# Kernel tuning notes

Hardware: AMD Instinct MI355X
Metric: run time of the kernel (lower is better)

## Reference

```python
import jax, jax.numpy as jnp
import numpy as np

HIDDEN = 2048
NUM_EXPERTS = 64
TOP_K = 2


def setup_inputs() -> dict:
    key = jax.random.key(0)
    k1, k2 = jax.random.split(key)
    x = jax.random.normal(k1, (4, 4096, HIDDEN), dtype=jnp.float32)
    # nn.Linear(hidden, num_experts, bias=False): weight shape [E, H], y = x @ W.T
    W = jax.random.normal(k2, (NUM_EXPERTS, HIDDEN), dtype=jnp.float32) * (HIDDEN ** -0.5)
    return {"x": x, "W": W}


def reference(x, W):
    B, S, H = x.shape
    E, K = NUM_EXPERTS, TOP_K
    xf = x.reshape(-1, H)                       # [N, H]
    gate_logits = xf @ W.T                      # [N, E]
    routing_probs = jax.nn.softmax(gate_logits, axis=-1)
    top_k_probs, top_k_indices = jax.lax.top_k(routing_probs, K)  # [N, K]
    denom = jnp.sum(top_k_probs, axis=-1, keepdims=True) + 1e-6
    routing_weights = (top_k_probs / denom).reshape(B, S, K)
    expert_indices = top_k_indices.reshape(B, S, K)

    # aux load-balancing loss (training path)
    N = xf.shape[0]
    # expert_mask.mean(0): fraction of tokens assigned to each expert
    assign_per_expert = jnp.zeros((E,), jnp.float32).at[top_k_indices.reshape(-1)].add(1.0) / N
    prob_per_expert = jnp.mean(routing_probs, axis=0)             # [E]
    aux_loss = (jnp.sum(prob_per_expert * prob_per_expert) * E
                + jnp.sum(assign_per_expert * assign_per_expert) * E)

    # expert_counts update (bincount over selected indices)
    expert_counts = jnp.zeros((E,), jnp.float32).at[top_k_indices.reshape(-1)].add(1.0)

    return routing_weights, expert_indices, aux_loss, expert_counts
```

## Files before the change

kernel.cpp:

```cpp
#include <hip/hip_runtime.h>

#define HID 2048
#define NEXP 64
#define NTOK 16384
#define TM 32
#define NTHREADS 256
#define NCHUNK 32
#define KPH 4
#define CPW 8
#define WS_W_OFF 1024
#define CHUNK_B 24576

#define OUT_IDX_OFF (2 * NTOK)
#define OUT_AUX_OFF (4 * NTOK)
#define OUT_CNT_OFF (4 * NTOK + 1)

typedef __attribute__((ext_vector_type(8))) short bhalf8;
typedef __attribute__((ext_vector_type(16))) float f32x16;

__device__ __forceinline__ void split3(float v, unsigned short& h1, unsigned short& h2, unsigned short& h3) {
    unsigned int u = __float_as_uint(v);
    unsigned int r1 = (u + 0x7FFFu + ((u >> 16) & 1u)) & 0xFFFF0000u;
    float f1 = __uint_as_float(r1);
    float d1 = v - f1;
    unsigned int u2 = __float_as_uint(d1);
    unsigned int r2 = (u2 + 0x7FFFu + ((u2 >> 16) & 1u)) & 0xFFFF0000u;
    float f2 = __uint_as_float(r2);
    float d2 = d1 - f2;
    h1 = (unsigned short)(r1 >> 16);
    h2 = (unsigned short)(r2 >> 16);
    h3 = (unsigned short)(__float_as_uint(d2) >> 16);
}

__device__ __forceinline__ void xsplit(float4 va, float4 vb, bhalf8& o1, bhalf8& o2, bhalf8& o3) {
    float f[8] = {va.x, va.y, va.z, va.w, vb.x, vb.y, vb.z, vb.w};
    union U { bhalf8 v; unsigned int u[4]; } u1, u2, u3;
#pragma unroll
    for (int t = 0; t < 4; t++) {
        float a = f[2 * t], b = f[2 * t + 1];
        unsigned int ua = __float_as_uint(a), ub = __float_as_uint(b);
        float da = a - __uint_as_float(ua & 0xFFFF0000u);
        float db = b - __uint_as_float(ub & 0xFFFF0000u);
        unsigned int uda = __float_as_uint(da), udb = __float_as_uint(db);
        float da2 = da - __uint_as_float(uda & 0xFFFF0000u);
        float db2 = db - __uint_as_float(udb & 0xFFFF0000u);
        u1.u[t] = (ua >> 16) | (ub & 0xFFFF0000u);
        u2.u[t] = (uda >> 16) | (udb & 0xFFFF0000u);
        u3.u[t] = (__float_as_uint(da2) >> 16) | (__float_as_uint(db2) & 0xFFFF0000u);
    }
    o1 = u1.v; o2 = u2.v; o3 = u3.v;
}

__global__ __launch_bounds__(256) void wsplit_kernel(const float* __restrict__ W,
                                                     char* __restrict__ wq,
                                                     float* __restrict__ wsf) {
    if (blockIdx.x == 0 && threadIdx.x < 2 * NEXP) wsf[threadIdx.x] = 0.f;
    int idx8 = (blockIdx.x * 256 + threadIdx.x) * 8;
    int e = idx8 >> 11;
    int k0 = idx8 & 2047;
    int c = k0 >> 6, ks = (k0 >> 4) & 3, half = (k0 >> 3) & 1;
    int g = e >> 5, l = (e & 31) + 32 * half;
    const float4* wp = (const float4*)(W + (size_t)e * HID + k0);
    float4 v0 = wp[0], v1 = wp[1];
    float f[8] = {v0.x, v0.y, v0.z, v0.w, v1.x, v1.y, v1.z, v1.w};
    unsigned int p1[4], p2[4], p3[4];
#pragma unroll
    for (int t = 0; t < 4; t++) {
        unsigned short a1, a2, a3, b1, b2, b3;
        split3(f[2 * t], a1, a2, a3);
        split3(f[2 * t + 1], b1, b2, b3);
        p1[t] = (unsigned int)a1 | ((unsigned int)b1 << 16);
        p2[t] = (unsigned int)a2 | ((unsigned int)b2 << 16);
        p3[t] = (unsigned int)a3 | ((unsigned int)b3 << 16);
    }
    char* base = wq + (size_t)(((c * 4 + ks) * 3 + 0) * 2 + g) * 1024 + l * 16;
    *(uint4*)(base)        = make_uint4(p1[0], p1[1], p1[2], p1[3]);
    *(uint4*)(base + 2048) = make_uint4(p2[0], p2[1], p2[2], p2[3]);
    *(uint4*)(base + 4096) = make_uint4(p3[0], p3[1], p3[2], p3[3]);
}

__global__ __launch_bounds__(NTHREADS, 2) void router_main(
    const float* __restrict__ x, const char* __restrict__ wq,
    float* __restrict__ out, float* __restrict__ ws_accum)
{
    __shared__ float slab[KPH * TM * 68];
    __shared__ float smax[TM];
    __shared__ float sinvZ[TM];
    __shared__ float scount[NEXP];

    const int tid = threadIdx.x;
    const int w = tid >> 6;
    const int lane = tid & 63;
    const int r = lane & 31;
    const int h = lane >> 5;
    const int n0 = blockIdx.x * TM;

    const float* xrow = x + (size_t)(n0 + r) * HID + h * 8;

    f32x16 acc0, acc1;
#pragma unroll
    for (int i = 0; i < 16; i++) { acc0[i] = 0.f; acc1[i] = 0.f; }

#pragma unroll 1
    for (int i = 0; i < CPW; ++i) {
        const int c = w * CPW + i;
        const float* xc = xrow + c * 64;
        float4 pxa[4], pxb[4];
#pragma unroll
        for (int ks = 0; ks < 4; ks++) {
            pxa[ks] = *(const float4*)(xc + ks * 16);
            pxb[ks] = *(const float4*)(xc + ks * 16 + 4);
        }
        const char* wc = wq + (size_t)c * CHUNK_B + lane * 16;
#pragma unroll
        for (int ks = 0; ks < 4; ks++) {
            bhalf8 A1, A2, A3;
            xsplit(pxa[ks], pxb[ks], A1, A2, A3);
            const char* wk = wc + ks * 6144;
            {
                bhalf8 B1 = *(const bhalf8*)(wk);
                bhalf8 B2 = *(const bhalf8*)(wk + 2048);
                bhalf8 B3 = *(const bhalf8*)(wk + 4096);
                acc0 = __builtin_amdgcn_mfma_f32_32x32x16_bf16(A1, B1, acc0, 0, 0, 0);
                acc0 = __builtin_amdgcn_mfma_f32_32x32x16_bf16(A1, B2, acc0, 0, 0, 0);
                acc0 = __builtin_amdgcn_mfma_f32_32x32x16_bf16(A2, B1, acc0, 0, 0, 0);
                acc0 = __builtin_amdgcn_mfma_f32_32x32x16_bf16(A1, B3, acc0, 0, 0, 0);
                acc0 = __builtin_amdgcn_mfma_f32_32x32x16_bf16(A2, B2, acc0, 0, 0, 0);
                acc0 = __builtin_amdgcn_mfma_f32_32x32x16_bf16(A3, B1, acc0, 0, 0, 0);
            }
            {
                bhalf8 B1 = *(const bhalf8*)(wk + 1024);
                bhalf8 B2 = *(const bhalf8*)(wk + 2048 + 1024);
                bhalf8 B3 = *(const bhalf8*)(wk + 4096 + 1024);
                acc1 = __builtin_amdgcn_mfma_f32_32x32x16_bf16(A1, B1, acc1, 0, 0, 0);
                acc1 = __builtin_amdgcn_mfma_f32_32x32x16_bf16(A1, B2, acc1, 0, 0, 0);
                acc1 = __builtin_amdgcn_mfma_f32_32x32x16_bf16(A2, B1, acc1, 0, 0, 0);
                acc1 = __builtin_amdgcn_mfma_f32_32x32x16_bf16(A1, B3, acc1, 0, 0, 0);
                acc1 = __builtin_amdgcn_mfma_f32_32x32x16_bf16(A2, B2, acc1, 0, 0, 0);
                acc1 = __builtin_amdgcn_mfma_f32_32x32x16_bf16(A3, B1, acc1, 0, 0, 0);
            }
        }
    }

#pragma unroll
    for (int reg = 0; reg < 16; reg++) {
        int row = (reg & 3) + 8 * (reg >> 2) + 4 * h;
        slab[(w * TM + row) * 68 + r]      = acc0[reg];
        slab[(w * TM + row) * 68 + 32 + r] = acc1[reg];
    }
    if (tid < NEXP) scount[tid] = 0.f;
    __syncthreads();

    float* logits = slab;
#pragma unroll
    for (int idx = tid; idx < TM * NEXP; idx += NTHREADS) {
        int t = idx >> 6, e = idx & 63;
        float v = slab[(0 * TM + t) * 68 + e] + slab[(1 * TM + t) * 68 + e]
                + slab[(2 * TM + t) * 68 + e] + slab[(3 * TM + t) * 68 + e];
        logits[t * 68 + e] = v;
    }
    __syncthreads();

    if (tid < TM) {
        const int t = tid;
        float m1 = -3.4e38f, m2 = -3.4e38f;
        int i1 = 0, i2 = 0;
        for (int e = 0; e < NEXP; e++) {
            float v = logits[t * 68 + e];
            if (v > m1) { m2 = m1; i2 = i1; m1 = v; i1 = e; }
            else if (v > m2) { m2 = v; i2 = e; }
        }
        float Z = 0.f;
        for (int e = 0; e < NEXP; e++)
            Z += __expf(logits[t * 68 + e] - m1);
        float invZ = 1.f / Z;
        float p1 = invZ;
        float p2 = __expf(m2 - m1) * invZ;
        float denom = p1 + p2 + 1e-6f;
        int n = n0 + t;
        out[2 * n + 0] = p1 / denom;
        out[2 * n + 1] = p2 / denom;
        out[OUT_IDX_OFF + 2 * n + 0] = (float)i1;
        out[OUT_IDX_OFF + 2 * n + 1] = (float)i2;
        smax[t] = m1;
        sinvZ[t] = invZ;
        atomicAdd(&scount[i1], 1.f);
        atomicAdd(&scount[i2], 1.f);
    }
    __syncthreads();

    if (tid < NEXP) {
        const int e = tid;
        float s = 0.f;
        for (int t = 0; t < TM; t++)
            s += __expf(logits[t * 68 + e] - smax[t]) * sinvZ[t];
        atomicAdd(&ws_accum[e], s);
        atomicAdd(&ws_accum[NEXP + e], scount[e]);
    }
}

__global__ void router_finish(const float* __restrict__ ws_accum,
                              float* __restrict__ out)
{
    const int e = threadIdx.x;
    const float invN = 1.f / (float)NTOK;
    float p = ws_accum[e] * invN;
    float a = ws_accum[NEXP + e] * invN;
    float v = p * p + a * a;
#pragma unroll
    for (int off = 32; off > 0; off >>= 1)
        v += __shfl_down(v, off);
    if (e == 0) out[OUT_AUX_OFF] = v * (float)NEXP;
    out[OUT_CNT_OFF + e] = ws_accum[NEXP + e];
}

extern "C" void kernel_launch(void* const* d_in, const int* in_sizes, int n_in,
                              void* d_out, int out_size, void* d_ws, size_t ws_size,
                              hipStream_t stream)
{
    const float* x = (const float*)d_in[0];
    const float* W = (const float*)d_in[1];
    float* out = (float*)d_out;
    float* wsf = (float*)d_ws;
    char* wq = (char*)d_ws + WS_W_OFF;

    wsplit_kernel<<<64, 256, 0, stream>>>(W, wq, wsf);
    router_main<<<NTOK / TM, NTHREADS, 0, stream>>>(x, wq, out, wsf);
    router_finish<<<1, 64, 0, stream>>>(wsf, out);
}
```

Baseline: 217.0 us.

## Split K across 8 waves and parallelize top-2 softmax with wave shuffles

The main router kernel now runs 512 threads per block, so each of 8 waves handles 4 of the 32 K-chunks instead of 8, and launch bounds request 4 blocks per CU. This doubles the waves working on each 32-token tile to hide global-load latency. The serial per-token top-2 and softmax loop, which ran on 32 threads, is replaced by 64-lane wave-shuffle reductions, and per-expert probability sums come from shared-memory atomics. The cost is a larger shared slab and a longer cross-wave partial-sum reduction, plus possible register pressure from the tighter launch bounds. The weight-split kernel is also relaunched as 256 blocks of 64 threads.

```diff
diff --git a/kernel.cpp b/kernel.cpp
--- a/kernel.cpp
+++ b/kernel.cpp
@@ -4,10 +4,11 @@
 #define NEXP 64
 #define NTOK 16384
 #define TM 32
-#define NTHREADS 256
+#define NTHREADS 512
 #define NCHUNK 32
-#define KPH 4
-#define CPW 8
+#define KPH 8
+#define CPW 4
+#define TPW 4
 #define WS_W_OFF 1024
 #define CHUNK_B 24576
 
@@ -51,11 +52,11 @@
     o1 = u1.v; o2 = u2.v; o3 = u3.v;
 }
 
-__global__ __launch_bounds__(256) void wsplit_kernel(const float* __restrict__ W,
-                                                     char* __restrict__ wq,
-                                                     float* __restrict__ wsf) {
-    if (blockIdx.x == 0 && threadIdx.x < 2 * NEXP) wsf[threadIdx.x] = 0.f;
-    int idx8 = (blockIdx.x * 256 + threadIdx.x) * 8;
+__global__ __launch_bounds__(64) void wsplit_kernel(const float* __restrict__ W,
+                                                    char* __restrict__ wq,
+                                                    float* __restrict__ wsf) {
+    if (blockIdx.x < 2) wsf[blockIdx.x * 64 + threadIdx.x] = 0.f;
+    int idx8 = (blockIdx.x * 64 + threadIdx.x) * 8;
     int e = idx8 >> 11;
     int k0 = idx8 & 2047;
     int c = k0 >> 6, ks = (k0 >> 4) & 3, half = (k0 >> 3) & 1;
@@ -79,14 +80,13 @@
     *(uint4*)(base + 4096) = make_uint4(p3[0], p3[1], p3[2], p3[3]);
 }
 
-__global__ __launch_bounds__(NTHREADS, 2) void router_main(
+__global__ __launch_bounds__(NTHREADS, 4) void router_main(
     const float* __restrict__ x, const char* __restrict__ wq,
     float* __restrict__ out, float* __restrict__ ws_accum)
 {
     __shared__ float slab[KPH * TM * 68];
-    __shared__ float smax[TM];
-    __shared__ float sinvZ[TM];
     __shared__ float scount[NEXP];
+    __shared__ float sprob[NEXP];
 
     const int tid = threadIdx.x;
     const int w = tid >> 6;
@@ -117,28 +117,24 @@
             bhalf8 A1, A2, A3;
             xsplit(pxa[ks], pxb[ks], A1, A2, A3);
             const char* wk = wc + ks * 6144;
-            {
-                bhalf8 B1 = *(const bhalf8*)(wk);
-                bhalf8 B2 = *(const bhalf8*)(wk + 2048);
-                bhalf8 B3 = *(const bhalf8*)(wk + 4096);
-                acc0 = __builtin_amdgcn_mfma_f32_32x32x16_bf16(A1, B1, acc0, 0, 0, 0);
-                acc0 = __builtin_amdgcn_mfma_f32_32x32x16_bf16(A1, B2, acc0, 0, 0, 0);
-                acc0 = __builtin_amdgcn_mfma_f32_32x32x16_bf16(A2, B1, acc0, 0, 0, 0);
-                acc0 = __builtin_amdgcn_mfma_f32_32x32x16_bf16(A1, B3, acc0, 0, 0, 0);
-                acc0 = __builtin_amdgcn_mfma_f32_32x32x16_bf16(A2, B2, acc0, 0, 0, 0);
-                acc0 = __builtin_amdgcn_mfma_f32_32x32x16_bf16(A3, B1, acc0, 0, 0, 0);
-            }
-            {
-                bhalf8 B1 = *(const bhalf8*)(wk + 1024);
-                bhalf8 B2 = *(const bhalf8*)(wk + 2048 + 1024);
-                bhalf8 B3 = *(const bhalf8*)(wk + 4096 + 1024);
-                acc1 = __builtin_amdgcn_mfma_f32_32x32x16_bf16(A1, B1, acc1, 0, 0, 0);
-                acc1 = __builtin_amdgcn_mfma_f32_32x32x16_bf16(A1, B2, acc1, 0, 0, 0);
-                acc1 = __builtin_amdgcn_mfma_f32_32x32x16_bf16(A2, B1, acc1, 0, 0, 0);
-                acc1 = __builtin_amdgcn_mfma_f32_32x32x16_bf16(A1, B3, acc1, 0, 0, 0);
-                acc1 = __builtin_amdgcn_mfma_f32_32x32x16_bf16(A2, B2, acc1, 0, 0, 0);
-                acc1 = __builtin_amdgcn_mfma_f32_32x32x16_bf16(A3, B1, acc1, 0, 0, 0);
-            }
+            bhalf8 B1 = *(const bhalf8*)(wk);
+            bhalf8 B2 = *(const bhalf8*)(wk + 2048);
+            bhalf8 B3 = *(const bhalf8*)(wk + 4096);
+            bhalf8 C1 = *(const bhalf8*)(wk + 1024);
+            bhalf8 C2 = *(const bhalf8*)(wk + 2048 + 1024);
+            bhalf8 C3 = *(const bhalf8*)(wk + 4096 + 1024);
+            acc0 = __builtin_amdgcn_mfma_f32_32x32x16_bf16(A1, B1, acc0, 0, 0, 0);
+            acc0 = __builtin_amdgcn_mfma_f32_32x32x16_bf16(A1, B2, acc0, 0, 0, 0);
+            acc0 = __builtin_amdgcn_mfma_f32_32x32x16_bf16(A2, B1, acc0, 0, 0, 0);
+            acc0 = __builtin_amdgcn_mfma_f32_32x32x16_bf16(A1, B3, acc0, 0, 0, 0);
+            acc0 = __builtin_amdgcn_mfma_f32_32x32x16_bf16(A2, B2, acc0, 0, 0, 0);
+            acc0 = __builtin_amdgcn_mfma_f32_32x32x16_bf16(A3, B1, acc0, 0, 0, 0);
+            acc1 = __builtin_amdgcn_mfma_f32_32x32x16_bf16(A1, C1, acc1, 0, 0, 0);
+            acc1 = __builtin_amdgcn_mfma_f32_32x32x16_bf16(A1, C2, acc1, 0, 0, 0);
+            acc1 = __builtin_amdgcn_mfma_f32_32x32x16_bf16(A2, C1, acc1, 0, 0, 0);
+            acc1 = __builtin_amdgcn_mfma_f32_32x32x16_bf16(A1, C3, acc1, 0, 0, 0);
+            acc1 = __builtin_amdgcn_mfma_f32_32x32x16_bf16(A2, C2, acc1, 0, 0, 0);
+            acc1 = __builtin_amdgcn_mfma_f32_32x32x16_bf16(A3, C1, acc1, 0, 0, 0);
         }
     }
 
@@ -148,54 +144,66 @@
         slab[(w * TM + row) * 68 + r]      = acc0[reg];
         slab[(w * TM + row) * 68 + 32 + r] = acc1[reg];
     }
-    if (tid < NEXP) scount[tid] = 0.f;
+    if (tid < NEXP) { scount[tid] = 0.f; sprob[tid] = 0.f; }
     __syncthreads();
 
     float* logits = slab;
 #pragma unroll
     for (int idx = tid; idx < TM * NEXP; idx += NTHREADS) {
         int t = idx >> 6, e = idx & 63;
-        float v = slab[(0 * TM + t) * 68 + e] + slab[(1 * TM + t) * 68 + e]
-                + slab[(2 * TM + t) * 68 + e] + slab[(3 * TM + t) * 68 + e];
+        float v = 0.f;
+#pragma unroll
+        for (int p = 0; p < KPH; p++) v += slab[(p * TM + t) * 68 + e];
         logits[t * 68 + e] = v;
     }
     __syncthreads();
 
-    if (tid < TM) {
-        const int t = tid;
-        float m1 = -3.4e38f, m2 = -3.4e38f;
-        int i1 = 0, i2 = 0;
-        for (int e = 0; e < NEXP; e++) {
-            float v = logits[t * 68 + e];
-            if (v > m1) { m2 = m1; i2 = i1; m1 = v; i1 = e; }
-            else if (v > m2) { m2 = v; i2 = e; }
-        }
-        float Z = 0.f;
-        for (int e = 0; e < NEXP; e++)
-            Z += __expf(logits[t * 68 + e] - m1);
+    float pacc = 0.f;
+#pragma unroll 1
+    for (int j = 0; j < TPW; j++) {
+        const int t = w * TPW + j;
+        const float v = logits[t * 68 + lane];
+        float m1 = v, m2 = -3.4e38f;
+        int i1 = lane, i2 = 0;
+#pragma unroll
+        for (int off = 32; off > 0; off >>= 1) {
+            float om1 = __shfl_xor(m1, off);
+            int   oi1 = __shfl_xor(i1, off);
+            float om2 = __shfl_xor(m2, off);
+            int   oi2 = __shfl_xor(i2, off);
+            if (om1 > m1 || (om1 == m1 && oi1 < i1)) {
+                if (m1 > om2 || (m1 == om2 && i1 < oi2)) { m2 = m1; i2 = i1; }
+                else { m2 = om2; i2 = oi2; }
+                m1 = om1; i1 = oi1;
+            } else {
+                if (om1 > m2 || (om1 == m2 && oi1 < i2)) { m2 = om1; i2 = oi1; }
+            }
+        }
+        float p = __expf(v - m1);
+        float Z = p;
+#pragma unroll
+        for (int off = 32; off > 0; off >>= 1) Z += __shfl_xor(Z, off);
         float invZ = 1.f / Z;
-        float p1 = invZ;
-        float p2 = __expf(m2 - m1) * invZ;
-        float denom = p1 + p2 + 1e-6f;
-        int n = n0 + t;
-        out[2 * n + 0] = p1 / denom;
-        out[2 * n + 1] = p2 / denom;
-        out[OUT_IDX_OFF + 2 * n + 0] = (float)i1;
-        out[OUT_IDX_OFF + 2 * n + 1] = (float)i2;
-        smax[t] = m1;
-        sinvZ[t] = invZ;
-        atomicAdd(&scount[i1], 1.f);
-        atomicAdd(&scount[i2], 1.f);
-    }
+        pacc += p * invZ;
+        if (lane == 0) {
+            float p1 = invZ;
+            float p2 = __expf(m2 - m1) * invZ;
+            float denom = p1 + p2 + 1e-6f;
+            int n = n0 + t;
+            out[2 * n + 0] = p1 / denom;
+            out[2 * n + 1] = p2 / denom;
+            out[OUT_IDX_OFF + 2 * n + 0] = (float)i1;
+            out[OUT_IDX_OFF + 2 * n + 1] = (float)i2;
+            atomicAdd(&scount[i1], 1.f);
+            atomicAdd(&scount[i2], 1.f);
+        }
+    }
+    atomicAdd(&sprob[lane], pacc);
     __syncthreads();
 
     if (tid < NEXP) {
-        const int e = tid;
-        float s = 0.f;
-        for (int t = 0; t < TM; t++)
-            s += __expf(logits[t * 68 + e] - smax[t]) * sinvZ[t];
-        atomicAdd(&ws_accum[e], s);
-        atomicAdd(&ws_accum[NEXP + e], scount[e]);
+        atomicAdd(&ws_accum[tid], sprob[tid]);
+        atomicAdd(&ws_accum[NEXP + tid], scount[tid]);
     }
 }
 
@@ -224,7 +232,7 @@
     float* wsf = (float*)d_ws;
     char* wq = (char*)d_ws + WS_W_OFF;
 
-    wsplit_kernel<<<64, 256, 0, stream>>>(W, wq, wsf);
+    wsplit_kernel<<<256, 64, 0, stream>>>(W, wq, wsf);
     router_main<<<NTOK / TM, NTHREADS, 0, stream>>>(x, wq, out, wsf);
     router_finish<<<1, 64, 0, stream>>>(wsf, out);
 }
```

New measurement: 217.8 us. No clear change (+0.3%).
